# Optimization experiments

Hardware: AMD Instinct MI355X
Metric: run time of the kernel (lower is better)

The kernel has to match this reference:

```python
import jax, jax.numpy as jnp
import numpy as np

MARGIN = 0.5
N_CLASSES = 100

def setup_inputs() -> dict:
    key = jax.random.key(0)
    k1, k2 = jax.random.split(key)
    n, d = 8192, 128
    inputs = jax.random.normal(k1, (n, d), dtype=jnp.float32)
    targets = jax.random.randint(k2, (n,), 0, N_CLASSES, dtype=jnp.int64)
    return {"inputs": inputs, "targets": targets}

def reference(inputs, targets):
    # pairwise squared euclidean distances: [n, n]
    sq = jnp.sum(inputs * inputs, axis=1)  # [n]
    dist = sq[:, None] + sq[None, :] - 2.0 * (inputs @ inputs.T)
    dist = jnp.maximum(dist, 0.0)
    # positive mask: same label (diagonal included, matching original)
    mask = targets[:, None] == targets[None, :]  # [n, n] bool
    big = jnp.float32(1e30)
    dist_ap = jnp.max(jnp.where(mask, dist, -big), axis=1)  # hardest positive per row
    dist_an = jnp.min(jnp.where(mask, big, dist), axis=1)   # hardest negative per row
    loss = jnp.sum(jax.nn.relu(dist_ap - dist_an + MARGIN))
    return loss
```

## Files before the change

### kernel.cpp

```cpp
#include <hip/hip_runtime.h>
#include <hip/hip_bf16.h>

#define D 128
#define MARGIN 0.5f
#define NSPLIT 16
#define JSPAN 512

typedef __attribute__((ext_vector_type(8))) short bf16x8;
typedef __attribute__((ext_vector_type(4))) float f32x4;

__global__ void prep_kernel(const float* __restrict__ x,
                            float* __restrict__ sq,
                            unsigned* __restrict__ ap,
                            unsigned* __restrict__ an,
                            __hip_bfloat16* __restrict__ xb,
                            float* __restrict__ out, int n) {
    int tid = threadIdx.x;
    int row = blockIdx.x * 4 + (tid >> 6);
    int lane = tid & 63;
    const float2* xr = (const float2*)(x + (size_t)row * D);
    float2 v = xr[lane];
    __hip_bfloat162 b2;
    b2.x = __float2bfloat16(v.x);
    b2.y = __float2bfloat16(v.y);
    ((__hip_bfloat162*)(xb + (size_t)row * D))[lane] = b2;
    float s = v.x * v.x + v.y * v.y;
    #pragma unroll
    for (int o = 32; o > 0; o >>= 1) s += __shfl_xor(s, o, 64);
    if (lane == 0) {
        sq[row] = s;
        ap[row] = 0u;
        an[row] = 0x7F800000u;
    }
    if (blockIdx.x == 0 && tid == 0) *out = 0.0f;
}

__launch_bounds__(256, 4)
__global__ void gram_kernel(const __hip_bfloat16* __restrict__ xb,
                            const float* __restrict__ sq,
                            const int* __restrict__ tgt,
                            unsigned* __restrict__ ap,
                            unsigned* __restrict__ an, int n) {
    __shared__ __align__(16) __hip_bfloat16 Bs[4][32 * D];
    __shared__ float sqs[JSPAN];
    __shared__ int   tgs[JSPAN];

    const int tid  = threadIdx.x;
    const int wid  = tid >> 6;
    const int lane = tid & 63;
    const int quad = lane >> 4;
    const int l    = lane & 15;
    const int i0   = blockIdx.x * 128;
    const int j0   = blockIdx.y * JSPAN;
    const int rowbase = i0 + wid * 32;

    bf16x8 afrag[2][4];
    {
        const __hip_bfloat16* abase = xb + (size_t)(rowbase + l) * D + quad * 8;
        #pragma unroll
        for (int mt = 0; mt < 2; ++mt)
            #pragma unroll
            for (int ks = 0; ks < 4; ++ks)
                afrag[mt][ks] = *(const bf16x8*)(abase + (size_t)mt * 16 * D + ks * 32);
    }

    int li[2][4];
    #pragma unroll
    for (int mt = 0; mt < 2; ++mt)
        #pragma unroll
        for (int reg = 0; reg < 4; ++reg)
            li[mt][reg] = tgt[rowbase + mt * 16 + quad * 4 + reg];

    float lap[8], lan[8];
    #pragma unroll
    for (int k = 0; k < 8; ++k) { lap[k] = -1e30f; lan[k] = 1e30f; }

    const char* xbb = (const char*)xb;

    #define PREF_HALF(h)                                                      \
        do {                                                                  \
            const int s_ = (h) & 3;                                           \
            _Pragma("unroll")                                                 \
            for (int i_ = 0; i_ < 2; ++i_) {                                  \
                int q_ = wid * 128 + i_ * 64 + lane;                          \
                int r_ = q_ >> 4;                                             \
                int c_ = (q_ & 15) ^ (r_ & 15);                               \
                const char* g_ = xbb + (size_t)(j0 + (h) * 32 + r_) * 256     \
                                     + (size_t)c_ * 16;                       \
                char* l_ = (char*)Bs + (size_t)s_ * 8192                      \
                         + (size_t)(wid * 128 + i_ * 64) * 16;                \
                __builtin_amdgcn_global_load_lds(                             \
                    (const __attribute__((address_space(1))) void*)g_,        \
                    (__attribute__((address_space(3))) void*)l_, 16, 0, 0);   \
            }                                                                 \
        } while (0)

    #define COMP_HALF(h)                                                      \
        do {                                                                  \
            const char* Bb_ = (const char*)Bs + (size_t)((h) & 3) * 8192;     \
            _Pragma("unroll")                                                 \
            for (int jt = 0; jt < 2; ++jt) {                                  \
                f32x4 acc0 = (f32x4){0.f, 0.f, 0.f, 0.f};                     \
                f32x4 acc1 = (f32x4){0.f, 0.f, 0.f, 0.f};                     \
                __builtin_amdgcn_s_setprio(1);                                \
                _Pragma("unroll")                                             \
                for (int ks = 0; ks < 4; ++ks) {                              \
                    int q = (jt * 16 + l) * 16 + ((ks * 4 + quad) ^ l);       \
                    bf16x8 bfr = *(const bf16x8*)(Bb_ + (size_t)q * 16);      \
                    acc0 = __builtin_amdgcn_mfma_f32_16x16x32_bf16(           \
                        afrag[0][ks], bfr, acc0, 0, 0, 0);                    \
                    acc1 = __builtin_amdgcn_mfma_f32_16x16x32_bf16(           \
                        afrag[1][ks], bfr, acc1, 0, 0, 0);                    \
                }                                                             \
                __builtin_amdgcn_s_setprio(0);                                \
                int jb_ = (h) * 32 + jt * 16;                                 \
                float sjc = sqs[jb_ + l];                                     \
                int   tjc = tgs[jb_ + l];                                     \
                _Pragma("unroll")                                             \
                for (int reg = 0; reg < 4; ++reg) {                           \
                    float t0 = fmaf(-2.0f, acc0[reg], sjc);                   \
                    float t1 = fmaf(-2.0f, acc1[reg], sjc);                   \
                    bool s0 = (li[0][reg] == tjc);                            \
                    bool s1 = (li[1][reg] == tjc);                            \
                    lap[reg]     = fmaxf(lap[reg],     s0 ? t0 : -1e30f);     \
                    lan[reg]     = fminf(lan[reg],     s0 ? 1e30f : t0);      \
                    lap[4 + reg] = fmaxf(lap[4 + reg], s1 ? t1 : -1e30f);     \
                    lan[4 + reg] = fminf(lan[4 + reg], s1 ? 1e30f : t1);      \
                }                                                             \
            }                                                                 \
        } while (0)

    PREF_HALF(0);
    PREF_HALF(1);
    PREF_HALF(2);
    sqs[tid]       = sq[j0 + tid];
    sqs[tid + 256] = sq[j0 + tid + 256];
    tgs[tid]       = tgt[j0 + tid];
    tgs[tid + 256] = tgt[j0 + tid + 256];
    asm volatile("s_waitcnt lgkmcnt(0)" ::: "memory");

    for (int h = 0; h < 14; ++h) {
        asm volatile("s_waitcnt vmcnt(4)" ::: "memory");
        __builtin_amdgcn_s_barrier();
        asm volatile("" ::: "memory");
        if (h < 13) PREF_HALF(h + 3);
        COMP_HALF(h);
    }
    asm volatile("s_waitcnt vmcnt(2)" ::: "memory");
    __builtin_amdgcn_s_barrier();
    asm volatile("" ::: "memory");
    COMP_HALF(14);
    asm volatile("s_waitcnt vmcnt(0)" ::: "memory");
    __builtin_amdgcn_s_barrier();
    asm volatile("" ::: "memory");
    COMP_HALF(15);

    #undef PREF_HALF
    #undef COMP_HALF

    #pragma unroll
    for (int mt = 0; mt < 2; ++mt)
        #pragma unroll
        for (int reg = 0; reg < 4; ++reg) {
            float p = lap[mt * 4 + reg], q = lan[mt * 4 + reg];
            #pragma unroll
            for (int o = 1; o < 16; o <<= 1) {
                p = fmaxf(p, __shfl_xor(p, o, 64));
                q = fminf(q, __shfl_xor(q, o, 64));
            }
            if (l == mt * 4 + reg) {
                int gi = rowbase + mt * 16 + quad * 4 + reg;
                float s = sq[gi];
                atomicMax(&ap[gi], __float_as_uint(fmaxf(s + p, 0.0f)));
                atomicMin(&an[gi], __float_as_uint(fmaxf(s + q, 0.0f)));
            }
        }
}

__global__ void final_kernel(const unsigned* __restrict__ ap,
                             const unsigned* __restrict__ an,
                             float* __restrict__ out, int n) {
    int i = blockIdx.x * blockDim.x + threadIdx.x;
    float v = 0.f;
    if (i < n) {
        float p = __uint_as_float(ap[i]);
        float q = __uint_as_float(an[i]);
        v = fmaxf(p - q + MARGIN, 0.0f);
    }
    #pragma unroll
    for (int o = 32; o > 0; o >>= 1) v += __shfl_xor(v, o, 64);
    __shared__ float ws[4];
    int lane = threadIdx.x & 63, w = threadIdx.x >> 6;
    if (lane == 0) ws[w] = v;
    __syncthreads();
    if (threadIdx.x == 0) atomicAdd(out, ws[0] + ws[1] + ws[2] + ws[3]);
}

extern "C" void kernel_launch(void* const* d_in, const int* in_sizes, int n_in,
                              void* d_out, int out_size, void* d_ws, size_t ws_size,
                              hipStream_t stream) {
    const float* x   = (const float*)d_in[0];
    const int*   tgt = (const int*)d_in[1];
    float* out = (float*)d_out;
    const int n = in_sizes[1];

    float*          sq = (float*)d_ws;
    unsigned*       ap = (unsigned*)((char*)d_ws + (size_t)n * 4);
    unsigned*       an = ap + n;
    __hip_bfloat16* xb = (__hip_bfloat16*)((char*)d_ws + (size_t)n * 12);

    prep_kernel<<<n / 4, 256, 0, stream>>>(x, sq, ap, an, xb, out, n);
    dim3 grid(n / 128, NSPLIT);
    gram_kernel<<<grid, 256, 0, stream>>>(xb, sq, tgt, ap, an, n);
    final_kernel<<<n / 256, 256, 0, stream>>>(ap, an, out, n);
}
```

Before: 86.67 us.

## Double rows per block to reuse each B tile across more MFMAs

Each wave now computes 64 rows instead of 32, so every B fragment read from LDS feeds four MFMAs instead of two, and each block covers 256 rows. This halves the number of blocks and the global/LDS traffic for B per unit of output. In exchange, register pressure roughly doubles, launch bounds drop to 2 blocks per CU, and there are fewer blocks to hide latency.

```diff
diff --git a/kernel.cpp b/kernel.cpp
--- a/kernel.cpp
+++ b/kernel.cpp
@@ -35,7 +35,7 @@
     if (blockIdx.x == 0 && tid == 0) *out = 0.0f;
 }
 
-__launch_bounds__(256, 4)
+__launch_bounds__(256, 2)
 __global__ void gram_kernel(const __hip_bfloat16* __restrict__ xb,
                             const float* __restrict__ sq,
                             const int* __restrict__ tgt,
@@ -50,30 +50,30 @@
     const int lane = tid & 63;
     const int quad = lane >> 4;
     const int l    = lane & 15;
-    const int i0   = blockIdx.x * 128;
+    const int i0   = blockIdx.x * 256;
     const int j0   = blockIdx.y * JSPAN;
-    const int rowbase = i0 + wid * 32;
-
-    bf16x8 afrag[2][4];
+    const int rowbase = i0 + wid * 64;
+
+    bf16x8 afrag[4][4];
     {
         const __hip_bfloat16* abase = xb + (size_t)(rowbase + l) * D + quad * 8;
         #pragma unroll
-        for (int mt = 0; mt < 2; ++mt)
+        for (int mt = 0; mt < 4; ++mt)
             #pragma unroll
             for (int ks = 0; ks < 4; ++ks)
                 afrag[mt][ks] = *(const bf16x8*)(abase + (size_t)mt * 16 * D + ks * 32);
     }
 
-    int li[2][4];
-    #pragma unroll
-    for (int mt = 0; mt < 2; ++mt)
+    int li[4][4];
+    #pragma unroll
+    for (int mt = 0; mt < 4; ++mt)
         #pragma unroll
         for (int reg = 0; reg < 4; ++reg)
             li[mt][reg] = tgt[rowbase + mt * 16 + quad * 4 + reg];
 
-    float lap[8], lan[8];
-    #pragma unroll
-    for (int k = 0; k < 8; ++k) { lap[k] = -1e30f; lan[k] = 1e30f; }
+    float lap[16], lan[16];
+    #pragma unroll
+    for (int k = 0; k < 16; ++k) { lap[k] = -1e30f; lan[k] = 1e30f; }
 
     const char* xbb = (const char*)xb;
 
@@ -100,32 +100,35 @@
             const char* Bb_ = (const char*)Bs + (size_t)((h) & 3) * 8192;     \
             _Pragma("unroll")                                                 \
             for (int jt = 0; jt < 2; ++jt) {                                  \
-                f32x4 acc0 = (f32x4){0.f, 0.f, 0.f, 0.f};                     \
-                f32x4 acc1 = (f32x4){0.f, 0.f, 0.f, 0.f};                     \
+                f32x4 acc[4];                                                 \
+                _Pragma("unroll")                                             \
+                for (int mt = 0; mt < 4; ++mt)                                \
+                    acc[mt] = (f32x4){0.f, 0.f, 0.f, 0.f};                    \
                 __builtin_amdgcn_s_setprio(1);                                \
                 _Pragma("unroll")                                             \
                 for (int ks = 0; ks < 4; ++ks) {                              \
                     int q = (jt * 16 + l) * 16 + ((ks * 4 + quad) ^ l);       \
                     bf16x8 bfr = *(const bf16x8*)(Bb_ + (size_t)q * 16);      \
-                    acc0 = __builtin_amdgcn_mfma_f32_16x16x32_bf16(           \
-                        afrag[0][ks], bfr, acc0, 0, 0, 0);                    \
-                    acc1 = __builtin_amdgcn_mfma_f32_16x16x32_bf16(           \
-                        afrag[1][ks], bfr, acc1, 0, 0, 0);                    \
+                    _Pragma("unroll")                                         \
+                    for (int mt = 0; mt < 4; ++mt)                            \
+                        acc[mt] = __builtin_amdgcn_mfma_f32_16x16x32_bf16(    \
+                            afrag[mt][ks], bfr, acc[mt], 0, 0, 0);            \
                 }                                                             \
                 __builtin_amdgcn_s_setprio(0);                                \
                 int jb_ = (h) * 32 + jt * 16;                                 \
                 float sjc = sqs[jb_ + l];                                     \
                 int   tjc = tgs[jb_ + l];                                     \
                 _Pragma("unroll")                                             \
-                for (int reg = 0; reg < 4; ++reg) {                           \
-                    float t0 = fmaf(-2.0f, acc0[reg], sjc);                   \
-                    float t1 = fmaf(-2.0f, acc1[reg], sjc);                   \
-                    bool s0 = (li[0][reg] == tjc);                            \
-                    bool s1 = (li[1][reg] == tjc);                            \
-                    lap[reg]     = fmaxf(lap[reg],     s0 ? t0 : -1e30f);     \
-                    lan[reg]     = fminf(lan[reg],     s0 ? 1e30f : t0);      \
-                    lap[4 + reg] = fmaxf(lap[4 + reg], s1 ? t1 : -1e30f);     \
-                    lan[4 + reg] = fminf(lan[4 + reg], s1 ? 1e30f : t1);      \
+                for (int mt = 0; mt < 4; ++mt) {                              \
+                    _Pragma("unroll")                                         \
+                    for (int reg = 0; reg < 4; ++reg) {                       \
+                        float t0 = fmaf(-2.0f, acc[mt][reg], sjc);            \
+                        bool s0 = (li[mt][reg] == tjc);                       \
+                        lap[mt * 4 + reg] =                                   \
+                            fmaxf(lap[mt * 4 + reg], s0 ? t0 : -1e30f);       \
+                        lan[mt * 4 + reg] =                                   \
+                            fminf(lan[mt * 4 + reg], s0 ? 1e30f : t0);        \
+                    }                                                         \
                 }                                                             \
             }                                                                 \
         } while (0)
@@ -159,7 +162,7 @@
     #undef COMP_HALF
 
     #pragma unroll
-    for (int mt = 0; mt < 2; ++mt)
+    for (int mt = 0; mt < 4; ++mt)
         #pragma unroll
         for (int reg = 0; reg < 4; ++reg) {
             float p = lap[mt * 4 + reg], q = lan[mt * 4 + reg];
@@ -210,7 +213,7 @@
     __hip_bfloat16* xb = (__hip_bfloat16*)((char*)d_ws + (size_t)n * 12);
 
     prep_kernel<<<n / 4, 256, 0, stream>>>(x, sq, ap, an, xb, out, n);
-    dim3 grid(n / 128, NSPLIT);
+    dim3 grid(n / 256, NSPLIT);
     gram_kernel<<<grid, 256, 0, stream>>>(xb, sq, tgt, ap, an, n);
     final_kernel<<<n / 256, 256, 0, stream>>>(ap, an, out, n);
 }
```

New measurement: 90.06 us. +3.9%, slower.

## Replace global atomics with per-split partial buffers and stagger wave LDS access order

Applied to the files above, without the earlier changes.

Each j-split block now writes its per-row hardest positive/negative to a dedicated partial buffer instead of issuing atomicMax/atomicMin, and the final kernel reduces across the NSPLIT partials. This removes atomic contention and the init stores in prep. Separately, the k-step and j-tile iteration order is rotated per wave so waves in a block read different LDS regions at the same time, aiming to reduce bank conflicts. It costs extra workspace and more reads in the final kernel.

```diff
diff --git a/kernel.cpp b/kernel.cpp
--- a/kernel.cpp
+++ b/kernel.cpp
@@ -11,8 +11,6 @@
 
 __global__ void prep_kernel(const float* __restrict__ x,
                             float* __restrict__ sq,
-                            unsigned* __restrict__ ap,
-                            unsigned* __restrict__ an,
                             __hip_bfloat16* __restrict__ xb,
                             float* __restrict__ out, int n) {
     int tid = threadIdx.x;
@@ -27,11 +25,7 @@
     float s = v.x * v.x + v.y * v.y;
     #pragma unroll
     for (int o = 32; o > 0; o >>= 1) s += __shfl_xor(s, o, 64);
-    if (lane == 0) {
-        sq[row] = s;
-        ap[row] = 0u;
-        an[row] = 0x7F800000u;
-    }
+    if (lane == 0) sq[row] = s;
     if (blockIdx.x == 0 && tid == 0) *out = 0.0f;
 }
 
@@ -39,8 +33,8 @@
 __global__ void gram_kernel(const __hip_bfloat16* __restrict__ xb,
                             const float* __restrict__ sq,
                             const int* __restrict__ tgt,
-                            unsigned* __restrict__ ap,
-                            unsigned* __restrict__ an, int n) {
+                            float* __restrict__ pap,
+                            float* __restrict__ pan, int n) {
     __shared__ __align__(16) __hip_bfloat16 Bs[4][32 * D];
     __shared__ float sqs[JSPAN];
     __shared__ int   tgs[JSPAN];
@@ -100,20 +94,22 @@
             const char* Bb_ = (const char*)Bs + (size_t)((h) & 3) * 8192;     \
             _Pragma("unroll")                                                 \
             for (int jt = 0; jt < 2; ++jt) {                                  \
+                const int jtr = jt ^ (wid & 1);                               \
                 f32x4 acc0 = (f32x4){0.f, 0.f, 0.f, 0.f};                     \
                 f32x4 acc1 = (f32x4){0.f, 0.f, 0.f, 0.f};                     \
                 __builtin_amdgcn_s_setprio(1);                                \
                 _Pragma("unroll")                                             \
                 for (int ks = 0; ks < 4; ++ks) {                              \
-                    int q = (jt * 16 + l) * 16 + ((ks * 4 + quad) ^ l);       \
+                    const int ksr = (ks + wid) & 3;                           \
+                    int q = (jtr * 16 + l) * 16 + ((ksr * 4 + quad) ^ l);     \
                     bf16x8 bfr = *(const bf16x8*)(Bb_ + (size_t)q * 16);      \
                     acc0 = __builtin_amdgcn_mfma_f32_16x16x32_bf16(           \
-                        afrag[0][ks], bfr, acc0, 0, 0, 0);                    \
+                        afrag[0][ksr], bfr, acc0, 0, 0, 0);                   \
                     acc1 = __builtin_amdgcn_mfma_f32_16x16x32_bf16(           \
-                        afrag[1][ks], bfr, acc1, 0, 0, 0);                    \
+                        afrag[1][ksr], bfr, acc1, 0, 0, 0);                   \
                 }                                                             \
                 __builtin_amdgcn_s_setprio(0);                                \
-                int jb_ = (h) * 32 + jt * 16;                                 \
+                int jb_ = (h) * 32 + jtr * 16;                                \
                 float sjc = sqs[jb_ + l];                                     \
                 int   tjc = tgs[jb_ + l];                                     \
                 _Pragma("unroll")                                             \
@@ -171,22 +167,23 @@
             if (l == mt * 4 + reg) {
                 int gi = rowbase + mt * 16 + quad * 4 + reg;
                 float s = sq[gi];
-                atomicMax(&ap[gi], __float_as_uint(fmaxf(s + p, 0.0f)));
-                atomicMin(&an[gi], __float_as_uint(fmaxf(s + q, 0.0f)));
+                pap[(size_t)blockIdx.y * n + gi] = fmaxf(s + p, 0.0f);
+                pan[(size_t)blockIdx.y * n + gi] = fmaxf(s + q, 0.0f);
             }
         }
 }
 
-__global__ void final_kernel(const unsigned* __restrict__ ap,
-                             const unsigned* __restrict__ an,
+__global__ void final_kernel(const float* __restrict__ pap,
+                             const float* __restrict__ pan,
                              float* __restrict__ out, int n) {
     int i = blockIdx.x * blockDim.x + threadIdx.x;
-    float v = 0.f;
-    if (i < n) {
-        float p = __uint_as_float(ap[i]);
-        float q = __uint_as_float(an[i]);
-        v = fmaxf(p - q + MARGIN, 0.0f);
+    float p = pap[i], q = pan[i];
+    #pragma unroll
+    for (int s = 1; s < NSPLIT; ++s) {
+        p = fmaxf(p, pap[(size_t)s * n + i]);
+        q = fminf(q, pan[(size_t)s * n + i]);
     }
+    float v = fmaxf(p - q + MARGIN, 0.0f);
     #pragma unroll
     for (int o = 32; o > 0; o >>= 1) v += __shfl_xor(v, o, 64);
     __shared__ float ws[4];
@@ -204,13 +201,13 @@
     float* out = (float*)d_out;
     const int n = in_sizes[1];
 
-    float*          sq = (float*)d_ws;
-    unsigned*       ap = (unsigned*)((char*)d_ws + (size_t)n * 4);
-    unsigned*       an = ap + n;
-    __hip_bfloat16* xb = (__hip_bfloat16*)((char*)d_ws + (size_t)n * 12);
-
-    prep_kernel<<<n / 4, 256, 0, stream>>>(x, sq, ap, an, xb, out, n);
+    float*          sq  = (float*)d_ws;
+    float*          pap = (float*)((char*)d_ws + (size_t)n * 4);
+    float*          pan = (float*)((char*)d_ws + (size_t)n * 4 + (size_t)n * NSPLIT * 4);
+    __hip_bfloat16* xb  = (__hip_bfloat16*)((char*)d_ws + (size_t)n * 4 + (size_t)n * NSPLIT * 8);
+
+    prep_kernel<<<n / 4, 256, 0, stream>>>(x, sq, xb, out, n);
     dim3 grid(n / 128, NSPLIT);
-    gram_kernel<<<grid, 256, 0, stream>>>(xb, sq, tgt, ap, an, n);
-    final_kernel<<<n / 256, 256, 0, stream>>>(ap, an, out, n);
-}
+    gram_kernel<<<grid, 256, 0, stream>>>(xb, sq, tgt, pap, pan, n);
+    final_kernel<<<n / 256, 256, 0, stream>>>(pap, pan, out, n);
+}
```

New measurement: 142.1 us. 63.9% more time.
